# Kernel optimization log

Hardware: AMD Instinct MI355X
Metric: run time of the kernel (lower is better)

The kernel has to match this reference:

```python
import jax, jax.numpy as jnp
import numpy as np

NEG_MIN = float(np.finfo(np.float32).min)
LN_EPS = 1e-05


def _layer_norm(x, g, b):
    m = jnp.mean(x, axis=-1, keepdims=True)
    v = jnp.var(x, axis=-1, keepdims=True)
    return (x - m) * jax.lax.rsqrt(v + LN_EPS) * g + b


def _rel_shift_uni(x):
    # x: [qlen, rlen, bsz, n_head] -- Transformer-XL relative shift
    q, r, b, n = x.shape
    zero_pad = jnp.zeros((q, 1, b, n), x.dtype)
    x_padded = jnp.concatenate([zero_pad, x], axis=1).reshape(r + 1, q, b, n)
    return x_padded[1:].reshape(q, r, b, n)


def setup_inputs() -> dict:
    key = jax.random.key(0)
    ks = jax.random.split(key, 12)
    qlen, bsz, d_model = 2048, 2, 1024
    n_head, d_head, d_inner = 16, 64, 4096

    w = jax.random.normal(ks[0], (qlen, bsz, d_model), dtype=jnp.float32)

    # sinusoidal relative position embedding, positions klen-1 .. 0
    pos_seq = jnp.arange(qlen - 1, -1, -1, dtype=jnp.float32)
    inv_freq = 1.0 / (10000.0 ** (jnp.arange(0, d_model, 2, dtype=jnp.float32) / d_model))
    sinusoid = pos_seq[:, None] * inv_freq[None, :]
    r = jnp.concatenate([jnp.sin(sinusoid), jnp.cos(sinusoid)], axis=-1)  # [qlen, d_model]

    s = 0.02
    r_w_bias = jax.random.normal(ks[1], (n_head, d_head), dtype=jnp.float32) * s
    r_r_bias = jax.random.normal(ks[2], (n_head, d_head), dtype=jnp.float32) * s
    qkv_w = jax.random.normal(ks[3], (d_model, 3 * n_head * d_head), dtype=jnp.float32) * s
    r_net_w = jax.random.normal(ks[4], (d_model, n_head * d_head), dtype=jnp.float32) * s
    o_w = jax.random.normal(ks[5], (n_head * d_head, d_model), dtype=jnp.float32) * s
    ffn_w1 = jax.random.normal(ks[6], (d_model, d_inner), dtype=jnp.float32) * s
    ffn_b1 = jnp.zeros((d_inner,), dtype=jnp.float32)
    ffn_w2 = jax.random.normal(ks[7], (d_inner, d_model), dtype=jnp.float32) * s
    ffn_b2 = jnp.zeros((d_model,), dtype=jnp.float32)
    ln1_g = jnp.ones((d_model,), dtype=jnp.float32)
    ln1_b = jnp.zeros((d_model,), dtype=jnp.float32)
    ln2_g = jnp.ones((d_model,), dtype=jnp.float32)
    ln2_b = jnp.zeros((d_model,), dtype=jnp.float32)

    # causal mask: position j > i is masked (uni-directional attention)
    attn_mask = jnp.triu(jnp.ones((qlen, qlen), dtype=bool), k=1)

    return {"w": w, "r": r, "r_w_bias": r_w_bias, "r_r_bias": r_r_bias,
            "attn_mask": attn_mask, "qkv_w": qkv_w, "r_net_w": r_net_w, "o_w": o_w,
            "ln1_g": ln1_g, "ln1_b": ln1_b, "ffn_w1": ffn_w1, "ffn_b1": ffn_b1,
            "ffn_w2": ffn_w2, "ffn_b2": ffn_b2, "ln2_g": ln2_g, "ln2_b": ln2_b}


def reference(w, r, r_w_bias, r_r_bias, attn_mask, qkv_w, r_net_w, o_w,
              ln1_g, ln1_b, ffn_w1, ffn_b1, ffn_w2, ffn_b2, ln2_g, ln2_b):
    qlen, bsz, d_model = w.shape
    n_head, d_head = r_w_bias.shape
    scale = 1.0 / (d_head ** 0.5)

    # qkv projection (post-lnorm path: no pre-norm)
    w_heads = w @ qkv_w  # [q, b, 3*n*d]
    w_q, w_k, w_v = jnp.split(w_heads, 3, axis=-1)
    w_q = w_q.reshape(qlen, bsz, n_head, d_head)
    w_k = w_k.reshape(qlen, bsz, n_head, d_head)
    w_v = w_v.reshape(qlen, bsz, n_head, d_head)

    r_k = (r @ r_net_w).reshape(r.shape[0], n_head, d_head)  # [rlen, n, d]

    # AC: content term, BD: position term with rel-shift
    AC = jnp.einsum('ibnd,jbnd->ijbn', w_q + r_w_bias, w_k)
    BD = jnp.einsum('ibnd,jnd->ijbn', w_q + r_r_bias, r_k)
    BD = _rel_shift_uni(BD)

    attn_score = (AC + BD) * scale
    attn_score = jnp.where(attn_mask[:, :, None, None], NEG_MIN, attn_score)
    attn_prob = jax.nn.softmax(attn_score, axis=1)  # softmax over key axis j

    attn_vec = jnp.einsum('ijbn,jbnd->ibnd', attn_prob, w_v)
    attn_vec = attn_vec.reshape(qlen, bsz, n_head * d_head)
    attn_out = attn_vec @ o_w

    x = _layer_norm(w + attn_out, ln1_g, ln1_b)  # post-lnorm

    # PositionwiseFF (post-lnorm, eval: dropout inactive)
    core = jax.nn.relu(x @ ffn_w1 + ffn_b1) @ ffn_w2 + ffn_b2
    out = _layer_norm(x + core, ln2_g, ln2_b)
    return out
```

## Files before the change

### kernel.cpp

```cpp
#include <hip/hip_runtime.h>
#include <math.h>


typedef __attribute__((ext_vector_type(8))) short short8;
typedef __attribute__((ext_vector_type(4))) float floatx4;

__device__ inline unsigned short f2bf(float f) {
  union { float f; unsigned u; } v; v.f = f;
  unsigned r = v.u + 0x7FFFu + ((v.u >> 16) & 1u);
  return (unsigned short)(r >> 16);
}
__device__ inline float bf2f(unsigned short u) {
  union { unsigned u; float f; } v; v.u = ((unsigned)u) << 16; return v.f;
}

#define G2L(gp, lp)                                                  \
  __builtin_amdgcn_global_load_lds(                                  \
      (const __attribute__((address_space(1))) void*)(gp),           \
      (__attribute__((address_space(3))) void*)(lp), 16, 0, 0)

__global__ __launch_bounds__(256) void prep_kernel(
    const float* __restrict__ w, unsigned short* __restrict__ wb,
    const float* __restrict__ r, unsigned short* __restrict__ rb,
    const float* __restrict__ qkv_w, unsigned short* __restrict__ qkvT,
    const float* __restrict__ r_net_w, unsigned short* __restrict__ rnetT,
    const float* __restrict__ o_w, unsigned short* __restrict__ owT,
    const float* __restrict__ ffn_w1, unsigned short* __restrict__ w1T,
    const float* __restrict__ ffn_w2, unsigned short* __restrict__ w2T) {
  __shared__ __align__(16) unsigned short Ts[64][68];
  const int blk = blockIdx.x;
  const int t = threadIdx.x;
  if (blk < 6144) {
    const float* in = blk < 4096 ? w : r;
    unsigned short* outp = blk < 4096 ? wb : rb;
    const int i = (blk < 4096 ? blk : blk - 4096) * 256 + t;
    float4 v = ((const float4*)in)[i];
    ((ushort4*)outp)[i] =
        make_ushort4(f2bf(v.x), f2bf(v.y), f2bf(v.z), f2bf(v.w));
    return;
  }
  const float* src; unsigned short* dst; int K, N, idx;
  if (blk < 6912)      { src = qkv_w;   dst = qkvT;  K = 1024; N = 3072; idx = blk - 6144; }
  else if (blk < 7168) { src = r_net_w; dst = rnetT; K = 1024; N = 1024; idx = blk - 6912; }
  else if (blk < 7424) { src = o_w;     dst = owT;   K = 1024; N = 1024; idx = blk - 7168; }
  else if (blk < 8448) { src = ffn_w1;  dst = w1T;   K = 1024; N = 4096; idx = blk - 7424; }
  else                 { src = ffn_w2;  dst = w2T;   K = 4096; N = 1024; idx = blk - 8448; }
  const int nbx = N >> 6;
  const int k0 = (idx / nbx) * 64, n0 = (idx % nbx) * 64;
  const int rr = t >> 4, c = (t & 15) * 4;
#pragma unroll
  for (int rb2 = 0; rb2 < 64; rb2 += 16) {
    float4 v = *(const float4*)(src + (size_t)(k0 + rb2 + rr) * N + n0 + c);
    *(ushort4*)&Ts[rb2 + rr][c] =
        make_ushort4(f2bf(v.x), f2bf(v.y), f2bf(v.z), f2bf(v.w));
  }
  __syncthreads();
#pragma unroll
  for (int rb2 = 0; rb2 < 64; rb2 += 16) {
    const int nn = rb2 + rr;
    ushort4 o = make_ushort4(Ts[c + 0][nn], Ts[c + 1][nn],
                             Ts[c + 2][nn], Ts[c + 3][nn]);
    *(ushort4*)(dst + (size_t)(n0 + nn) * K + k0 + c) = o;
  }
}

template<int BIAS, int RELU, int OUT_BF16>
__device__ __forceinline__ void bgemm_body(
    const unsigned short* __restrict__ A, const unsigned short* __restrict__ Bt,
    const float* __restrict__ bias, void* __restrict__ C,
    int M, int N, int Kstride, int Klen, size_t psize,
    int bx, int by, int kz,
    unsigned short* As, unsigned short* Bs) {
  const int t = threadIdx.x;
  const int wv = t >> 6, lane = t & 63, quad = lane >> 4, lq = lane & 15;
  const int m0 = by * 128, n0 = bx * 128;
  const int wvm = (wv >> 1) * 64, wvn = (wv & 1) * 64;

  const int srow = t >> 2;
  const int scol = (t & 3) * 8;
  const size_t koff = (size_t)kz * Klen;
  const unsigned short* Ag = A + (size_t)(m0 + srow) * Kstride + scol + koff;
  const unsigned short* Bg = Bt + (size_t)(n0 + srow) * Kstride + scol + koff;
  unsigned short* AsW0 = As + (size_t)wv * 512;
  unsigned short* AsW1 = As + 4096 + (size_t)wv * 512;
  unsigned short* BsW0 = Bs + (size_t)wv * 512;
  unsigned short* BsW1 = Bs + 4096 + (size_t)wv * 512;

  floatx4 acc[4][4];
#pragma unroll
  for (int am = 0; am < 4; ++am)
#pragma unroll
    for (int bn = 0; bn < 4; ++bn) acc[am][bn] = (floatx4){0.f, 0.f, 0.f, 0.f};

  for (int k0 = 0; k0 < Klen; k0 += 64) {
    __syncthreads();
    G2L(Ag + k0, AsW0);
    G2L(Ag + (size_t)64 * Kstride + k0, AsW0 + 64 * 32);
    G2L(Ag + k0 + 32, AsW1);
    G2L(Ag + (size_t)64 * Kstride + k0 + 32, AsW1 + 64 * 32);
    G2L(Bg + k0, BsW0);
    G2L(Bg + (size_t)64 * Kstride + k0, BsW0 + 64 * 32);
    G2L(Bg + k0 + 32, BsW1);
    G2L(Bg + (size_t)64 * Kstride + k0 + 32, BsW1 + 64 * 32);
    __syncthreads();

#pragma unroll
    for (int s = 0; s < 2; ++s) {
      const unsigned short* Asub = s ? As + 4096 : As;
      const unsigned short* Bsub = s ? Bs + 4096 : Bs;
      short8 af[4], bf[4];
#pragma unroll
      for (int am = 0; am < 4; ++am)
        af[am] = *(const short8*)&Asub[(wvm + am * 16 + lq) * 32 + quad * 8];
#pragma unroll
      for (int bn = 0; bn < 4; ++bn)
        bf[bn] = *(const short8*)&Bsub[(wvn + bn * 16 + lq) * 32 + quad * 8];
#pragma unroll
      for (int am = 0; am < 4; ++am)
#pragma unroll
        for (int bn = 0; bn < 4; ++bn)
          acc[am][bn] = __builtin_amdgcn_mfma_f32_16x16x32_bf16(
              af[am], bf[bn], acc[am][bn], 0, 0, 0);
    }
  }

  float bs[4] = {0.f, 0.f, 0.f, 0.f};
  if (BIAS) {
    if (kz == 0) {
#pragma unroll
      for (int bn = 0; bn < 4; ++bn) bs[bn] = bias[n0 + wvn + bn * 16 + lq];
    }
  }
  float* Cf = (float*)C + (size_t)kz * psize;
#pragma unroll
  for (int am = 0; am < 4; ++am) {
#pragma unroll
    for (int u = 0; u < 4; ++u) {
      const size_t row = m0 + wvm + am * 16 + quad * 4 + u;
#pragma unroll
      for (int bn = 0; bn < 4; ++bn) {
        const size_t col = n0 + wvn + bn * 16 + lq;
        float v = acc[am][bn][u];
        if (BIAS) v += bs[bn];
        if (RELU) v = fmaxf(v, 0.f);
        if (OUT_BF16) ((unsigned short*)C)[row * N + col] = f2bf(v);
        else          Cf[row * N + col] = v;
      }
    }
  }
}

template<int BIAS, int RELU, int OUT_BF16>
__global__ __launch_bounds__(256) void bgemm_kernel(
    const unsigned short* __restrict__ A, const unsigned short* __restrict__ Bt,
    const float* __restrict__ bias, void* __restrict__ C,
    int M, int N, int Kstride, int Klen, size_t psize) {
  __shared__ __align__(16) unsigned short As[2 * 128 * 32];
  __shared__ __align__(16) unsigned short Bs[2 * 128 * 32];
  bgemm_body<BIAS, RELU, OUT_BF16>(A, Bt, bias, C, M, N, Kstride, Klen, psize,
                                   blockIdx.x, blockIdx.y, blockIdx.z, As, Bs);
}

template<int BIAS, int RELU, int OUT_BF16>
__device__ __forceinline__ void gemm256p8_body(
    const unsigned short* __restrict__ A, const unsigned short* __restrict__ Bt,
    const float* __restrict__ bias, void* __restrict__ C,
    int N, int K, int bx, int by,
    unsigned short* As0, unsigned short* Bs0,
    unsigned short* As1, unsigned short* Bs1) {
  const int t = threadIdx.x;
  const int wv = t >> 6, lane = t & 63, quad = lane >> 4, lq = lane & 15;
  const int wr = wv >> 2, wc = wv & 3;
  const int m0 = by * 256, n0 = bx * 256;

  const int srow = t >> 3;
  const int scol = ((t & 7) * 8) ^ ((t & 32) >> 1);
  const unsigned short* Ag = A + (size_t)(m0 + srow) * K + scol;
  const unsigned short* Bg = Bt + (size_t)(n0 + srow) * K + scol;
  const int c0 = (quad * 8) ^ ((lq & 4) << 2);

  floatx4 acc[8][4];
#pragma unroll
  for (int am = 0; am < 8; ++am)
#pragma unroll
    for (int bn = 0; bn < 4; ++bn) acc[am][bn] = (floatx4){0.f, 0.f, 0.f, 0.f};

  short8 af[8], bfA[4], bfB[4];

#define STG(dst, gp, rbase, kofs)                                            \
  do {                                                                       \
    G2L((gp) + (size_t)(rbase) * K + (kofs), (dst) + (rbase) * 64 + wv * 512); \
    G2L((gp) + (size_t)((rbase) + 64) * K + (kofs),                          \
        (dst) + ((rbase) + 64) * 64 + wv * 512);                             \
  } while (0)

#define LDAF(buf, ah)                                                        \
  _Pragma("unroll")                                                          \
  for (int i_ = 0; i_ < 4; ++i_) {                                           \
    const int ar_ = (wr * 128 + (ah) * 64 + i_ * 16 + lq) * 64;              \
    af[i_ * 2 + 0] = *(const short8*)&(buf)[ar_ + c0];                       \
    af[i_ * 2 + 1] = *(const short8*)&(buf)[ar_ + 32 + c0];                  \
  }

#define LDBF(dst, buf, bh)                                                   \
  _Pragma("unroll")                                                          \
  for (int i_ = 0; i_ < 2; ++i_) {                                           \
    const int br_ = (wc * 64 + (bh) * 32 + i_ * 16 + lq) * 64;               \
    dst[i_ * 2 + 0] = *(const short8*)&(buf)[br_ + c0];                      \
    dst[i_ * 2 + 1] = *(const short8*)&(buf)[br_ + 32 + c0];                 \
  }

#define MM(ah, bh, bfX)                                                      \
  __builtin_amdgcn_s_setprio(1);                                             \
  _Pragma("unroll")                                                          \
  for (int i_ = 0; i_ < 4; ++i_)                                             \
    _Pragma("unroll")                                                        \
    for (int j_ = 0; j_ < 2; ++j_) {                                         \
      acc[(ah) * 4 + i_][(bh) * 2 + j_] =                                    \
          __builtin_amdgcn_mfma_f32_16x16x32_bf16(                           \
              af[i_ * 2 + 0], bfX[j_ * 2 + 0],                               \
              acc[(ah) * 4 + i_][(bh) * 2 + j_], 0, 0, 0);                   \
      acc[(ah) * 4 + i_][(bh) * 2 + j_] =                                    \
          __builtin_amdgcn_mfma_f32_16x16x32_bf16(                           \
              af[i_ * 2 + 1], bfX[j_ * 2 + 1],                               \
              acc[(ah) * 4 + i_][(bh) * 2 + j_], 0, 0, 0);                   \
    }                                                                        \
  __builtin_amdgcn_s_setprio(0);

#define BAR() __builtin_amdgcn_s_barrier()
#define VM2() asm volatile("s_waitcnt vmcnt(2)" ::: "memory")
#define VM0() asm volatile("s_waitcnt vmcnt(0)" ::: "memory")

  const int NI = K >> 7;

  STG(As0, Ag, 0, 0);   STG(Bs0, Bg, 0, 0);
  STG(As0, Ag, 128, 0); STG(Bs0, Bg, 128, 0);
  STG(As1, Ag, 0, 64);
  VM2();
  BAR();

  for (int it = 0; it < NI; ++it) {
    const int ke = it * 128;
    const bool stg = (it + 1 < NI);

    LDAF(As0, 0); LDBF(bfA, Bs0, 0);
    STG(Bs1, Bg, 0, ke + 64);
    BAR(); MM(0, 0, bfA); BAR();
    LDBF(bfB, Bs0, 1);
    STG(As1, Ag, 128, ke + 64);
    BAR(); MM(0, 1, bfB); BAR();
    LDAF(As0, 1);
    STG(Bs1, Bg, 128, ke + 64);
    BAR(); MM(1, 1, bfB); BAR();
    if (stg) STG(As0, Ag, 0, ke + 128);
    BAR(); MM(1, 0, bfA);
    if (stg) VM2(); else VM0();
    BAR();
    LDAF(As1, 0); LDBF(bfA, Bs1, 0);
    if (stg) STG(Bs0, Bg, 0, ke + 128);
    BAR(); MM(0, 0, bfA); BAR();
    LDBF(bfB, Bs1, 1);
    if (stg) STG(As0, Ag, 128, ke + 128);
    BAR(); MM(0, 1, bfB); BAR();
    LDAF(As1, 1);
    if (stg) STG(Bs0, Bg, 128, ke + 128);
    BAR(); MM(1, 1, bfB); BAR();
    if (stg) STG(As1, Ag, 0, ke + 192);
    BAR(); MM(1, 0, bfA);
    if (stg) VM2(); else VM0();
    BAR();
  }

#undef STG
#undef LDAF
#undef LDBF
#undef MM
#undef BAR
#undef VM2
#undef VM0

  float bs[4] = {0.f, 0.f, 0.f, 0.f};
  if (BIAS) {
#pragma unroll
    for (int bn = 0; bn < 4; ++bn) bs[bn] = bias[n0 + wc * 64 + bn * 16 + lq];
  }
#pragma unroll
  for (int am = 0; am < 8; ++am) {
#pragma unroll
    for (int u = 0; u < 4; ++u) {
      const size_t row = m0 + wr * 128 + am * 16 + quad * 4 + u;
#pragma unroll
      for (int bn = 0; bn < 4; ++bn) {
        const size_t col = n0 + wc * 64 + bn * 16 + lq;
        float v = acc[am][bn][u];
        if (BIAS) v += bs[bn];
        if (RELU) v = fmaxf(v, 0.f);
        if (OUT_BF16) ((unsigned short*)C)[row * N + col] = f2bf(v);
        else          ((float*)C)[row * N + col] = v;
      }
    }
  }
}

template<int BIAS, int RELU, int OUT_BF16>
__global__ __launch_bounds__(512, 2) void gemm256p8_kernel(
    const unsigned short* __restrict__ A, const unsigned short* __restrict__ Bt,
    const float* __restrict__ bias, void* __restrict__ C, int N, int K) {
  __shared__ __align__(16) unsigned short As[2][256 * 64];
  __shared__ __align__(16) unsigned short Bs[2][256 * 64];
  gemm256p8_body<BIAS, RELU, OUT_BF16>(A, Bt, bias, C, N, K,
                                       blockIdx.x, blockIdx.y,
                                       As[0], Bs[0], As[1], Bs[1]);
}

__global__ __launch_bounds__(512, 2) void qkv_rk256_kernel(
    const unsigned short* __restrict__ wb, const unsigned short* __restrict__ qkvT,
    unsigned short* __restrict__ w_heads,
    const unsigned short* __restrict__ rbf, const unsigned short* __restrict__ rnetT,
    unsigned short* __restrict__ rk) {
  __shared__ __align__(16) unsigned short As[2][256 * 64];
  __shared__ __align__(16) unsigned short Bs[2][256 * 64];
  const int bid = blockIdx.x;
  if (bid < 192) {
    gemm256p8_body<0, 0, 1>(wb, qkvT, nullptr, w_heads, 3072, 1024,
                            bid % 12, bid / 12, As[0], Bs[0], As[1], Bs[1]);
  } else {
    const int b2 = bid - 192;
    gemm256p8_body<0, 0, 1>(rbf, rnetT, nullptr, rk, 1024, 1024,
                            b2 % 4, b2 / 4, As[0], Bs[0], As[1], Bs[1]);
  }
}

__global__ __launch_bounds__(512, 4) void attn_mfma_kernel(
    const unsigned short* __restrict__ w_heads,
    const unsigned short* __restrict__ r_k,
    const float* __restrict__ r_w_bias, const float* __restrict__ r_r_bias,
    unsigned short* __restrict__ attn_vec) {
  __shared__ __align__(16) unsigned short Ks[64 * 72];
  __shared__ __align__(16) unsigned short Vt[64 * 72];
  __shared__ __align__(16) unsigned short Rb[256 * 72];
  __shared__ __align__(16) unsigned short Pl[8 * 16 * 72];

  const int t = threadIdx.x;
  const int wv = t >> 6, lane = t & 63, quad = lane >> 4, lq = lane & 15;
  const int g = blockIdx.x;
  const int qq = g >> 5, bnb = g & 31;
  const int it = (qq < 8) ? (15 - qq) : (qq - 8);
  const int b = bnb & 1, n = bnb >> 1;
  const int i0 = it * 128, iw = i0 + wv * 16;

  const int kr = t >> 3, kc8 = (t & 7) * 8;
  const int vj = t & 31, vc = (t >> 5) * 4;

  short8 qw[2], qr[2];
  {
    const unsigned short* qrow =
        w_heads + (size_t)((iw + lq) * 2 + b) * 3072 + n * 64;
    short8 a0 = *(const short8*)(qrow + quad * 8);
    short8 a1 = *(const short8*)(qrow + 32 + quad * 8);
    const float* wbp = r_w_bias + n * 64;
    const float* rbp = r_r_bias + n * 64;
#pragma unroll
    for (int j = 0; j < 8; ++j) {
      const int k0 = quad * 8 + j, k1 = 32 + quad * 8 + j;
      const float q0 = bf2f((unsigned short)a0[j]);
      const float q1 = bf2f((unsigned short)a1[j]);
      qw[0][j] = (short)f2bf(q0 + wbp[k0]);
      qr[0][j] = (short)f2bf(q0 + rbp[k0]);
      qw[1][j] = (short)f2bf(q1 + wbp[k1]);
      qr[1][j] = (short)f2bf(q1 + rbp[k1]);
    }
  }

  floatx4 o[4];
#pragma unroll
  for (int dt = 0; dt < 4; ++dt) o[dt] = (floatx4){0.f, 0.f, 0.f, 0.f};
  float lrow[4] = {0.f, 0.f, 0.f, 0.f};

  unsigned short* Pw = Pl + wv * (16 * 72);
  const int wb2 = 112 - wv * 16;

  int g_idx[4]; bool g_hi[4];
#pragma unroll
  for (int u = 0; u < 4; ++u) {
    const int s = 15 - (quad * 4 + u);
    g_idx[u] = quad * 16 + ((s + lq) & 15);
    g_hi[u] = (s + lq) >= 16;
  }

  const int pbase0 = 1920 - i0;
  const int jt_end = 2 * it + 2;

#pragma unroll
  for (int bq = 0; bq < 2; ++bq) {
    const int row = pbase0 + bq * 64 + kr;
    const int slot = row & 255;
    *(short8*)&Rb[slot * 72 + kc8] =
        *(const short8*)(r_k + (size_t)row * 1024 + n * 64 + kc8);
  }
  short8 sK, sR;
  ushort4 sVl, sVh;
  {
    const unsigned short* kb =
        w_heads + (size_t)(kr * 2 + b) * 3072 + n * 64 + 1024 + kc8;
    sK = *(const short8*)kb;
    const unsigned short* vbp =
        w_heads + (size_t)((2 * vj) * 2 + b) * 3072 + n * 64 + 2048 + vc;
    sVl = *(const ushort4*)vbp;
    sVh = *(const ushort4*)(vbp + 2 * 3072);
    int pg = pbase0 + 128 + kr; if (pg > 2047) pg = 2047;
    sR = *(const short8*)(r_k + (size_t)pg * 1024 + n * 64 + kc8);
  }

  for (int jt = 0; jt < jt_end; ++jt) {
    const int j0 = jt * 64;
    const int pbase = pbase0 + 64 * jt;

    asm volatile("" ::: "memory");
    __builtin_amdgcn_s_barrier();
    asm volatile("" ::: "memory");

    *(short8*)&Ks[kr * 72 + kc8] = sK;
#pragma unroll
    for (int i2 = 0; i2 < 4; ++i2)
      *(unsigned*)&Vt[(vc + i2) * 72 + 2 * vj] =
          (unsigned)sVl[i2] | ((unsigned)sVh[i2] << 16);
    {
      const int slot = (pbase + 128 + kr) & 255;
      *(short8*)&Rb[slot * 72 + kc8] = sR;
    }

    if (jt + 1 < jt_end) {
      const int j0n = j0 + 64;
      const unsigned short* kb =
          w_heads + (size_t)((j0n + kr) * 2 + b) * 3072 + n * 64 + 1024 + kc8;
      sK = *(const short8*)kb;
      const unsigned short* vbp =
          w_heads + (size_t)((j0n + 2 * vj) * 2 + b) * 3072 + n * 64 + 2048 + vc;
      sVl = *(const ushort4*)vbp;
      sVh = *(const ushort4*)(vbp + 2 * 3072);
      int pg = pbase + 192 + kr; if (pg > 2047) pg = 2047;
      sR = *(const short8*)(r_k + (size_t)pg * 1024 + n * 64 + kc8);
    }

    asm volatile("s_waitcnt lgkmcnt(0)" ::: "memory");
    __builtin_amdgcn_s_barrier();
    asm volatile("" ::: "memory");

    floatx4 ac[4];
#pragma unroll
    for (int ct = 0; ct < 4; ++ct) {
      short8 b0 = *(const short8*)&Ks[(ct * 16 + lq) * 72 + quad * 8];
      short8 b1 = *(const short8*)&Ks[(ct * 16 + lq) * 72 + 32 + quad * 8];
      floatx4 z = (floatx4){0.f, 0.f, 0.f, 0.f};
      z = __builtin_amdgcn_mfma_f32_16x16x32_bf16(qw[0], b0, z, 0, 0, 0);
      z = __builtin_amdgcn_mfma_f32_16x16x32_bf16(qw[1], b1, z, 0, 0, 0);
      ac[ct] = z;
    }
    floatx4 Tt[5];
#pragma unroll
    for (int pt = 0; pt < 5; ++pt) {
      const int slot = (pbase + wb2 + pt * 16 + lq) & 255;
      short8 b0 = *(const short8*)&Rb[slot * 72 + quad * 8];
      short8 b1 = *(const short8*)&Rb[slot * 72 + 32 + quad * 8];
      floatx4 z = (floatx4){0.f, 0.f, 0.f, 0.f};
      z = __builtin_amdgcn_mfma_f32_16x16x32_bf16(qr[0], b0, z, 0, 0, 0);
      z = __builtin_amdgcn_mfma_f32_16x16x32_bf16(qr[1], b1, z, 0, 0, 0);
      Tt[pt] = z;
    }

    const bool interior = (j0 + 63 <= iw);
    if (interior) {
#pragma unroll
      for (int u = 0; u < 4; ++u) {
        const int r = quad * 4 + u;
        float sh[5];
#pragma unroll
        for (int pt = 0; pt < 5; ++pt) sh[pt] = __shfl(Tt[pt][u], g_idx[u]);
#pragma unroll
        for (int ct = 0; ct < 4; ++ct) {
          const float bd = g_hi[u] ? sh[ct + 1] : sh[ct];
          const float xs = (ac[ct][u] + bd) * 0.18033688011112042f;
          float pr; asm("v_exp_f32 %0, %1" : "=v"(pr) : "v"(xs));
          Pw[r * 72 + ct * 16 + lq] = f2bf(pr);
          lrow[u] += pr;
        }
      }
    } else {
#pragma unroll
      for (int u = 0; u < 4; ++u) {
        const int r = quad * 4 + u, i = iw + r;
        float sh[5];
#pragma unroll
        for (int pt = 0; pt < 5; ++pt) sh[pt] = __shfl(Tt[pt][u], g_idx[u]);
#pragma unroll
        for (int ct = 0; ct < 4; ++ct) {
          const float bd = g_hi[u] ? sh[ct + 1] : sh[ct];
          const int j = j0 + ct * 16 + lq;
          const float xs = (ac[ct][u] + bd) * 0.18033688011112042f;
          float pr; asm("v_exp_f32 %0, %1" : "=v"(pr) : "v"(xs));
          pr = (j <= i) ? pr : 0.f;
          Pw[r * 72 + ct * 16 + lq] = f2bf(pr);
          lrow[u] += pr;
        }
      }
    }

    __builtin_amdgcn_s_waitcnt(0xC07F);

    short8 pA0 = *(const short8*)&Pw[lq * 72 + quad * 8];
    short8 pA1 = *(const short8*)&Pw[lq * 72 + 32 + quad * 8];
#pragma unroll
    for (int dt = 0; dt < 4; ++dt) {
      short8 v0 = *(const short8*)&Vt[(dt * 16 + lq) * 72 + quad * 8];
      short8 v1 = *(const short8*)&Vt[(dt * 16 + lq) * 72 + 32 + quad * 8];
      o[dt] = __builtin_amdgcn_mfma_f32_16x16x32_bf16(pA0, v0, o[dt], 0, 0, 0);
      o[dt] = __builtin_amdgcn_mfma_f32_16x16x32_bf16(pA1, v1, o[dt], 0, 0, 0);
    }
  }

#pragma unroll
  for (int u = 0; u < 4; ++u) {
    float l = lrow[u];
    l += __shfl_xor(l, 1);
    l += __shfl_xor(l, 2);
    l += __shfl_xor(l, 4);
    l += __shfl_xor(l, 8);
    const float linv = 1.f / l;
    const int i = iw + quad * 4 + u;
    unsigned short* op = attn_vec + (size_t)(i * 2 + b) * 1024 + n * 64 + lq;
#pragma unroll
    for (int dt = 0; dt < 4; ++dt) op[dt * 16] = f2bf(o[dt][u] * linv);
  }
}

__global__ __launch_bounds__(256) void ln_res_kernel(
    const float* __restrict__ X, const float* __restrict__ R0,
    const float* __restrict__ R1,
    const float* __restrict__ g, const float* __restrict__ bta,
    float* __restrict__ out, unsigned short* __restrict__ out_bf) {
  const int row = blockIdx.x;
  const int t = threadIdx.x;
  float4 xv = ((const float4*)(X + (size_t)row * 1024))[t];
  float4 rv = ((const float4*)(R0 + (size_t)row * 1024))[t];
  float4 v = make_float4(xv.x + rv.x, xv.y + rv.y, xv.z + rv.z, xv.w + rv.w);
  if (R1) {
    float4 r2 = ((const float4*)(R1 + (size_t)row * 1024))[t];
    v.x += r2.x; v.y += r2.y; v.z += r2.z; v.w += r2.w;
  }
  float s  = v.x + v.y + v.z + v.w;
  float sq = v.x * v.x + v.y * v.y + v.z * v.z + v.w * v.w;
#pragma unroll
  for (int off = 32; off > 0; off >>= 1) {
    s  += __shfl_xor(s, off);
    sq += __shfl_xor(sq, off);
  }
  __shared__ float ss[4], ssq[4];
  const int wid = t >> 6;
  if ((t & 63) == 0) { ss[wid] = s; ssq[wid] = sq; }
  __syncthreads();
  s  = ss[0] + ss[1] + ss[2] + ss[3];
  sq = ssq[0] + ssq[1] + ssq[2] + ssq[3];
  const float mean = s * (1.f / 1024.f);
  const float var  = sq * (1.f / 1024.f) - mean * mean;
  const float inv  = rsqrtf(var + 1e-5f);
  float4 gv = ((const float4*)g)[t];
  float4 bv = ((const float4*)bta)[t];
  float4 ov = make_float4((v.x - mean) * inv * gv.x + bv.x,
                          (v.y - mean) * inv * gv.y + bv.y,
                          (v.z - mean) * inv * gv.z + bv.z,
                          (v.w - mean) * inv * gv.w + bv.w);
  ((float4*)(out + (size_t)row * 1024))[t] = ov;
  if (out_bf)
    ((ushort4*)(out_bf + (size_t)row * 1024))[t] =
        make_ushort4(f2bf(ov.x), f2bf(ov.y), f2bf(ov.z), f2bf(ov.w));
}

extern "C" void kernel_launch(void* const* d_in, const int* in_sizes, int n_in,
                              void* d_out, int out_size, void* d_ws, size_t ws_size,
                              hipStream_t stream) {
  (void)in_sizes; (void)n_in; (void)out_size; (void)ws_size;
  const float* w        = (const float*)d_in[0];
  const float* r        = (const float*)d_in[1];
  const float* r_w_bias = (const float*)d_in[2];
  const float* r_r_bias = (const float*)d_in[3];
  const float* qkv_w    = (const float*)d_in[5];
  const float* r_net_w  = (const float*)d_in[6];
  const float* o_w      = (const float*)d_in[7];
  const float* ln1_g    = (const float*)d_in[8];
  const float* ln1_b    = (const float*)d_in[9];
  const float* ffn_w1   = (const float*)d_in[10];
  const float* ffn_b1   = (const float*)d_in[11];
  const float* ffn_w2   = (const float*)d_in[12];
  const float* ffn_b2   = (const float*)d_in[13];
  const float* ln2_g    = (const float*)d_in[14];
  const float* ln2_b    = (const float*)d_in[15];
  float* out = (float*)d_out;

  char* base = (char*)d_ws;
  const size_t MB = (size_t)1 << 20;
  unsigned short* w_heads = (unsigned short*)(base + 0);
  float*          aout0   = (float*)(base + 0);
  float*          aout1   = (float*)(base + 16 * MB);
  unsigned short* h1      = (unsigned short*)(base + 0);
  float*          x       = (float*)(base + 32 * MB);
  unsigned short* w2T     = (unsigned short*)(base + 48 * MB);
  unsigned short* w1T     = (unsigned short*)(base + 56 * MB);
  float*          core0   = (float*)(base + 56 * MB);
  float*          core1   = (float*)(base + 72 * MB);
  unsigned short* wb      = (unsigned short*)(base + 64 * MB);
  unsigned short* avec    = (unsigned short*)(base + 64 * MB);
  unsigned short* rb      = (unsigned short*)(base + 72 * MB);
  unsigned short* xb      = (unsigned short*)(base + 72 * MB);
  unsigned short* rk      = (unsigned short*)(base + 76 * MB);
  unsigned short* qkvT    = (unsigned short*)(base + 80 * MB);
  unsigned short* owT     = (unsigned short*)(base + 86 * MB);
  unsigned short* rnetT   = (unsigned short*)(base + 88 * MB);

  dim3 blk(256);
  prep_kernel<<<9472, blk, 0, stream>>>(w, wb, r, rb, qkv_w, qkvT,
                                        r_net_w, rnetT, o_w, owT,
                                        ffn_w1, w1T, ffn_w2, w2T);

  qkv_rk256_kernel<<<224, 512, 0, stream>>>(wb, qkvT, w_heads, rb, rnetT, rk);
  attn_mfma_kernel<<<512, 512, 0, stream>>>(
      w_heads, rk, r_w_bias, r_r_bias, avec);
  bgemm_kernel<0, 0, 0><<<dim3(8, 32, 2), blk, 0, stream>>>(
      avec, owT, nullptr, aout0, 4096, 1024, 1024, 512, (size_t)4096 * 1024);
  ln_res_kernel<<<4096, blk, 0, stream>>>(w, aout0, aout1, ln1_g, ln1_b, x, xb);
  gemm256p8_kernel<1, 1, 1><<<dim3(16, 16), 512, 0, stream>>>(
      xb, w1T, ffn_b1, h1, 4096, 1024);
  bgemm_kernel<1, 0, 0><<<dim3(8, 32, 2), blk, 0, stream>>>(
      h1, w2T, ffn_b2, core0, 4096, 1024, 4096, 2048, (size_t)4096 * 1024);
  ln_res_kernel<<<4096, blk, 0, stream>>>(x, core0, core1, ln2_g, ln2_b, out, nullptr);
}
```

Measured before the change: 413.1 us.

## Use 256x256 split-K-by-4 GEMM for FFN2 and raise MFMA priority in attention

The second FFN GEMM moves from the 128-tile bgemm with split-K 2 to the 256x256 pipelined GEMM with split-K 4. Its four fp32 partials are summed inside the residual layernorm kernel. This path only runs when the workspace is at least 120 MB, otherwise the old path is used. Separately, s_setprio raises wave priority around the MFMA blocks in the attention kernel. In exchange there are more partial buffers to write and read back, and the new path depends on workspace size.

```diff
diff --git a/kernel.cpp b/kernel.cpp
--- a/kernel.cpp
+++ b/kernel.cpp
@@ -165,7 +165,7 @@
 __device__ __forceinline__ void gemm256p8_body(
     const unsigned short* __restrict__ A, const unsigned short* __restrict__ Bt,
     const float* __restrict__ bias, void* __restrict__ C,
-    int N, int K, int bx, int by,
+    int N, int Kstride, int Klen, int bx, int by,
     unsigned short* As0, unsigned short* Bs0,
     unsigned short* As1, unsigned short* Bs1) {
   const int t = threadIdx.x;
@@ -175,8 +175,8 @@
 
   const int srow = t >> 3;
   const int scol = ((t & 7) * 8) ^ ((t & 32) >> 1);
-  const unsigned short* Ag = A + (size_t)(m0 + srow) * K + scol;
-  const unsigned short* Bg = Bt + (size_t)(n0 + srow) * K + scol;
+  const unsigned short* Ag = A + (size_t)(m0 + srow) * Kstride + scol;
+  const unsigned short* Bg = Bt + (size_t)(n0 + srow) * Kstride + scol;
   const int c0 = (quad * 8) ^ ((lq & 4) << 2);
 
   floatx4 acc[8][4];
@@ -189,8 +189,9 @@
 
 #define STG(dst, gp, rbase, kofs)                                            \
   do {                                                                       \
-    G2L((gp) + (size_t)(rbase) * K + (kofs), (dst) + (rbase) * 64 + wv * 512); \
-    G2L((gp) + (size_t)((rbase) + 64) * K + (kofs),                          \
+    G2L((gp) + (size_t)(rbase) * Kstride + (kofs),                           \
+        (dst) + (rbase) * 64 + wv * 512);                                    \
+    G2L((gp) + (size_t)((rbase) + 64) * Kstride + (kofs),                    \
         (dst) + ((rbase) + 64) * 64 + wv * 512);                             \
   } while (0)
 
@@ -231,7 +232,7 @@
 #define VM2() asm volatile("s_waitcnt vmcnt(2)" ::: "memory")
 #define VM0() asm volatile("s_waitcnt vmcnt(0)" ::: "memory")
 
-  const int NI = K >> 7;
+  const int NI = Klen >> 7;
 
   STG(As0, Ag, 0, 0);   STG(Bs0, Bg, 0, 0);
   STG(As0, Ag, 128, 0); STG(Bs0, Bg, 128, 0);
@@ -280,7 +281,7 @@
 #undef VM0
 
   float bs[4] = {0.f, 0.f, 0.f, 0.f};
-  if (BIAS) {
+  if (BIAS && bias) {
 #pragma unroll
     for (int bn = 0; bn < 4; ++bn) bs[bn] = bias[n0 + wc * 64 + bn * 16 + lq];
   }
@@ -308,9 +309,23 @@
     const float* __restrict__ bias, void* __restrict__ C, int N, int K) {
   __shared__ __align__(16) unsigned short As[2][256 * 64];
   __shared__ __align__(16) unsigned short Bs[2][256 * 64];
-  gemm256p8_body<BIAS, RELU, OUT_BF16>(A, Bt, bias, C, N, K,
+  gemm256p8_body<BIAS, RELU, OUT_BF16>(A, Bt, bias, C, N, K, K,
                                        blockIdx.x, blockIdx.y,
                                        As[0], Bs[0], As[1], Bs[1]);
+}
+
+template<int BIAS, int RELU>
+__global__ __launch_bounds__(512, 2) void gemm256p8_splitk_kernel(
+    const unsigned short* __restrict__ A, const unsigned short* __restrict__ Bt,
+    const float* __restrict__ bias, float* __restrict__ C,
+    int N, int Kstride, int Klen, size_t psize) {
+  __shared__ __align__(16) unsigned short As[2][256 * 64];
+  __shared__ __align__(16) unsigned short Bs[2][256 * 64];
+  const int kz = blockIdx.z;
+  gemm256p8_body<BIAS, RELU, 0>(A + (size_t)kz * Klen, Bt + (size_t)kz * Klen,
+                                kz == 0 ? bias : nullptr, C + kz * psize,
+                                N, Kstride, Klen, blockIdx.x, blockIdx.y,
+                                As[0], Bs[0], As[1], Bs[1]);
 }
 
 __global__ __launch_bounds__(512, 2) void qkv_rk256_kernel(
@@ -322,11 +337,11 @@
   __shared__ __align__(16) unsigned short Bs[2][256 * 64];
   const int bid = blockIdx.x;
   if (bid < 192) {
-    gemm256p8_body<0, 0, 1>(wb, qkvT, nullptr, w_heads, 3072, 1024,
+    gemm256p8_body<0, 0, 1>(wb, qkvT, nullptr, w_heads, 3072, 1024, 1024,
                             bid % 12, bid / 12, As[0], Bs[0], As[1], Bs[1]);
   } else {
     const int b2 = bid - 192;
-    gemm256p8_body<0, 0, 1>(rbf, rnetT, nullptr, rk, 1024, 1024,
+    gemm256p8_body<0, 0, 1>(rbf, rnetT, nullptr, rk, 1024, 1024, 1024,
                             b2 % 4, b2 / 4, As[0], Bs[0], As[1], Bs[1]);
   }
 }
@@ -447,6 +462,7 @@
     __builtin_amdgcn_s_barrier();
     asm volatile("" ::: "memory");
 
+    __builtin_amdgcn_s_setprio(1);
     floatx4 ac[4];
 #pragma unroll
     for (int ct = 0; ct < 4; ++ct) {
@@ -468,6 +484,7 @@
       z = __builtin_amdgcn_mfma_f32_16x16x32_bf16(qr[1], b1, z, 0, 0, 0);
       Tt[pt] = z;
     }
+    __builtin_amdgcn_s_setprio(0);
 
     const bool interior = (j0 + 63 <= iw);
     if (interior) {
@@ -510,6 +527,7 @@
 
     short8 pA0 = *(const short8*)&Pw[lq * 72 + quad * 8];
     short8 pA1 = *(const short8*)&Pw[lq * 72 + 32 + quad * 8];
+    __builtin_amdgcn_s_setprio(1);
 #pragma unroll
     for (int dt = 0; dt < 4; ++dt) {
       short8 v0 = *(const short8*)&Vt[(dt * 16 + lq) * 72 + quad * 8];
@@ -517,6 +535,7 @@
       o[dt] = __builtin_amdgcn_mfma_f32_16x16x32_bf16(pA0, v0, o[dt], 0, 0, 0);
       o[dt] = __builtin_amdgcn_mfma_f32_16x16x32_bf16(pA1, v1, o[dt], 0, 0, 0);
     }
+    __builtin_amdgcn_s_setprio(0);
   }
 
 #pragma unroll
@@ -536,7 +555,8 @@
 
 __global__ __launch_bounds__(256) void ln_res_kernel(
     const float* __restrict__ X, const float* __restrict__ R0,
-    const float* __restrict__ R1,
+    const float* __restrict__ R1, const float* __restrict__ R2,
+    const float* __restrict__ R3,
     const float* __restrict__ g, const float* __restrict__ bta,
     float* __restrict__ out, unsigned short* __restrict__ out_bf) {
   const int row = blockIdx.x;
@@ -546,6 +566,14 @@
   float4 v = make_float4(xv.x + rv.x, xv.y + rv.y, xv.z + rv.z, xv.w + rv.w);
   if (R1) {
     float4 r2 = ((const float4*)(R1 + (size_t)row * 1024))[t];
+    v.x += r2.x; v.y += r2.y; v.z += r2.z; v.w += r2.w;
+  }
+  if (R2) {
+    float4 r2 = ((const float4*)(R2 + (size_t)row * 1024))[t];
+    v.x += r2.x; v.y += r2.y; v.z += r2.z; v.w += r2.w;
+  }
+  if (R3) {
+    float4 r2 = ((const float4*)(R3 + (size_t)row * 1024))[t];
     v.x += r2.x; v.y += r2.y; v.z += r2.z; v.w += r2.w;
   }
   float s  = v.x + v.y + v.z + v.w;
@@ -579,7 +607,7 @@
 extern "C" void kernel_launch(void* const* d_in, const int* in_sizes, int n_in,
                               void* d_out, int out_size, void* d_ws, size_t ws_size,
                               hipStream_t stream) {
-  (void)in_sizes; (void)n_in; (void)out_size; (void)ws_size;
+  (void)in_sizes; (void)n_in; (void)out_size;
   const float* w        = (const float*)d_in[0];
   const float* r        = (const float*)d_in[1];
   const float* r_w_bias = (const float*)d_in[2];
@@ -608,6 +636,8 @@
   unsigned short* w1T     = (unsigned short*)(base + 56 * MB);
   float*          core0   = (float*)(base + 56 * MB);
   float*          core1   = (float*)(base + 72 * MB);
+  float*          core2   = (float*)(base + 88 * MB);
+  float*          core3   = (float*)(base + 104 * MB);
   unsigned short* wb      = (unsigned short*)(base + 64 * MB);
   unsigned short* avec    = (unsigned short*)(base + 64 * MB);
   unsigned short* rb      = (unsigned short*)(base + 72 * MB);
@@ -617,6 +647,8 @@
   unsigned short* owT     = (unsigned short*)(base + 86 * MB);
   unsigned short* rnetT   = (unsigned short*)(base + 88 * MB);
 
+  const bool big_ws = ws_size >= (size_t)120 * MB;
+
   dim3 blk(256);
   prep_kernel<<<9472, blk, 0, stream>>>(w, wb, r, rb, qkv_w, qkvT,
                                         r_net_w, rnetT, o_w, owT,
@@ -627,10 +659,19 @@
       w_heads, rk, r_w_bias, r_r_bias, avec);
   bgemm_kernel<0, 0, 0><<<dim3(8, 32, 2), blk, 0, stream>>>(
       avec, owT, nullptr, aout0, 4096, 1024, 1024, 512, (size_t)4096 * 1024);
-  ln_res_kernel<<<4096, blk, 0, stream>>>(w, aout0, aout1, ln1_g, ln1_b, x, xb);
+  ln_res_kernel<<<4096, blk, 0, stream>>>(w, aout0, aout1, nullptr, nullptr,
+                                          ln1_g, ln1_b, x, xb);
   gemm256p8_kernel<1, 1, 1><<<dim3(16, 16), 512, 0, stream>>>(
       xb, w1T, ffn_b1, h1, 4096, 1024);
-  bgemm_kernel<1, 0, 0><<<dim3(8, 32, 2), blk, 0, stream>>>(
-      h1, w2T, ffn_b2, core0, 4096, 1024, 4096, 2048, (size_t)4096 * 1024);
-  ln_res_kernel<<<4096, blk, 0, stream>>>(x, core0, core1, ln2_g, ln2_b, out, nullptr);
-}
+  if (big_ws) {
+    gemm256p8_splitk_kernel<1, 0><<<dim3(4, 16, 4), 512, 0, stream>>>(
+        h1, w2T, ffn_b2, core0, 1024, 4096, 1024, (size_t)4096 * 1024);
+    ln_res_kernel<<<4096, blk, 0, stream>>>(x, core0, core1, core2, core3,
+                                            ln2_g, ln2_b, out, nullptr);
+  } else {
+    bgemm_kernel<1, 0, 0><<<dim3(8, 32, 2), blk, 0, stream>>>(
+        h1, w2T, ffn_b2, core0, 4096, 1024, 4096, 2048, (size_t)4096 * 1024);
+    ln_res_kernel<<<4096, blk, 0, stream>>>(x, core0, core1, nullptr, nullptr,
+                                            ln2_g, ln2_b, out, nullptr);
+  }
+}
```

New measurement: 419.7 us. About the same (+1.6%).
